# Kernel optimization log

Measured on AMD Instinct MI355X. Metric: run time of the kernel, lower is better.

Reference implementation:

```python
import jax, jax.numpy as jnp
import numpy as np

BETA = 0.25

def setup_inputs() -> dict:
    key = jax.random.key(0)
    k1, k2 = jax.random.split(key)
    N, K, D = 262144, 1024, 64
    z = jax.random.normal(k1, (N, D), dtype=jnp.float32)
    codebook = jax.random.normal(k2, (K, D), dtype=jnp.float32)
    return {"z": z, "codebook": codebook}

def reference(z, codebook):
    # Squared Euclidean distances (argmin identical to torch.cdist argmin):
    # ||z||^2 - 2 z.C^T + ||C||^2 , shape [N, K]
    z_sq = jnp.sum(z * z, axis=1, keepdims=True)            # [N,1]
    c_sq = jnp.sum(codebook * codebook, axis=1)             # [K]
    dist = z_sq - 2.0 * (z @ codebook.T) + c_sq[None, :]    # [N,K]
    indices = jnp.argmin(dist, axis=1)                      # [N] int
    z_q = codebook[indices]                                 # [N,D]
    codebook_loss = jnp.mean((jax.lax.stop_gradient(z_q) - z) ** 2)
    commitment_loss = jnp.mean((z_q - jax.lax.stop_gradient(z)) ** 2)
    vq_loss = codebook_loss + BETA * commitment_loss
    z_q_st = z + jax.lax.stop_gradient(z_q - z)             # straight-through
    return (z_q_st, vq_loss, indices, z_q)
```

## Files before the change

### kernel.cpp

```cpp
#include <hip/hip_runtime.h>
#include <hip/hip_bf16.h>

typedef __bf16 bf16x8 __attribute__((ext_vector_type(8)));
typedef float  f32x4  __attribute__((ext_vector_type(4)));

static constexpr int N_ROWS  = 262144;
static constexpr int K_CODES = 1024;
static constexpr int D_DIM   = 64;

static constexpr long LOSS_OFF = (long)N_ROWS * D_DIM;
static constexpr long IDX_OFF  = LOSS_OFF + 1;
static constexpr long ZQ_OFF   = IDX_OFF + N_ROWS;

static constexpr size_t CSQ_B   = 0;
static constexpr size_t BFRAG_B = 4096;
static constexpr size_t CNT_B   = BFRAG_B + (size_t)16 * 16384;
static constexpr size_t LIST_B  = CNT_B + 256;
static constexpr size_t PART_B  = LIST_B + (size_t)N_ROWS * 4;
static constexpr size_t WS_NEEDED = PART_B + (size_t)16384 * 4;

static constexpr int   EPI_BLOCKS = (N_ROWS * D_DIM) / (256 * 4);
static constexpr float MARGIN = 0.05f;

#define GLOAD_LDS16(g, l) __builtin_amdgcn_global_load_lds( \
    (const __attribute__((address_space(1))) unsigned int*)(g), \
    (__attribute__((address_space(3))) unsigned int*)(l), 16, 0, 0)

__global__ __launch_bounds__(256) void csq_kernel(const float* __restrict__ cb,
                                                  float* __restrict__ ws) {
    int g = blockIdx.x * 256 + threadIdx.x;
    const float4* row = reinterpret_cast<const float4*>(cb) + (size_t)g * (D_DIM / 4);
    float s = 0.f;
    #pragma unroll
    for (int j = 0; j < D_DIM / 4; ++j) {
        float4 v = row[j];
        s = fmaf(v.x, v.x, s); s = fmaf(v.y, v.y, s);
        s = fmaf(v.z, v.z, s); s = fmaf(v.w, v.w, s);
    }
    ws[g] = s;
}

__global__ __launch_bounds__(256) void prep_kernel(const float* __restrict__ cb,
                                                   char* __restrict__ wsb) {
    int t = blockIdx.x * 256 + threadIdx.x;
    int c  = t >> 3;
    int ks = (t >> 2) & 1;
    int g  = t & 3;
    const float* src = cb + (size_t)c * 64 + ks * 32 + g * 8;
    float f[8];
    #pragma unroll
    for (int i = 0; i < 8; ++i) f[i] = src[i];
    bf16x8 h, l;
    #pragma unroll
    for (int i = 0; i < 8; ++i) {
        __bf16 hv = (__bf16)f[i];
        h[i] = hv;
        l[i] = (__bf16)(f[i] - (float)hv);
    }
    int tile = c >> 6, cf = (c >> 4) & 3, n = c & 15;
    int lane = g * 16 + n;
    char* base = wsb + BFRAG_B + (size_t)tile * 16384;
    *reinterpret_cast<bf16x8*>(base + ((0 * 2 + ks) * 4 + cf) * 1024 + lane * 16) = h;
    *reinterpret_cast<bf16x8*>(base + ((1 * 2 + ks) * 4 + cf) * 1024 + lane * 16) = l;
}

__global__ __launch_bounds__(256, 2) void vq_gemm_kernel(const float* __restrict__ z,
                                                         char* __restrict__ wsb,
                                                         float* __restrict__ out) {
    __shared__ __align__(16) unsigned char sbuf[2 * 16384 + 4096];
    float* lds_csq = (float*)(sbuf + 32768);

    const int tid  = threadIdx.x;
    const int lane = tid & 63, wid = tid >> 6;
    const int l15  = lane & 15, lg = lane >> 4;

    const float* csq = (const float*)(wsb + CSQ_B);
    #pragma unroll
    for (int i = 0; i < 4; ++i) lds_csq[tid + 256 * i] = csq[tid + 256 * i];

    const int rowbase = blockIdx.x * 256 + wid * 64;
    bf16x8 ah[4][2], al[4][2];
    #pragma unroll
    for (int rf = 0; rf < 4; ++rf) {
        const float* zr = z + (size_t)(rowbase + rf * 16 + l15) * 64 + lg * 8;
        #pragma unroll
        for (int ks = 0; ks < 2; ++ks) {
            float4 a = *reinterpret_cast<const float4*>(zr + ks * 32);
            float4 b = *reinterpret_cast<const float4*>(zr + ks * 32 + 4);
            float f[8] = {a.x, a.y, a.z, a.w, b.x, b.y, b.z, b.w};
            bf16x8 h, l;
            #pragma unroll
            for (int i = 0; i < 8; ++i) {
                __bf16 hv = (__bf16)f[i];
                h[i] = hv;
                l[i] = (__bf16)(f[i] - (float)hv);
            }
            ah[rf][ks] = h; al[rf][ks] = l;
        }
    }

    float m1[16], m2[16]; int i1[16];
    #pragma unroll
    for (int s = 0; s < 16; ++s) { m1[s] = INFINITY; m2[s] = INFINITY; i1[s] = 0; }

    const char* bsrc = wsb + BFRAG_B;

    auto stage = [&](int buf, int t) {
        const char* src = bsrc + (size_t)t * 16384;
        #pragma unroll
        for (int it = 0; it < 4; ++it) {
            GLOAD_LDS16(src + it * 4096 + wid * 1024 + lane * 16,
                        sbuf + buf * 16384 + it * 4096 + wid * 1024);
        }
    };

    stage(0, 0);
    __syncthreads();

    for (int t = 0; t < 16; ++t) {
        if (t < 15) stage((t + 1) & 1, t + 1);
        const unsigned char* B = sbuf + (t & 1) * 16384;
        #pragma unroll
        for (int cf = 0; cf < 4; ++cf) {
            bf16x8 bh0 = *reinterpret_cast<const bf16x8*>(B + (0 * 4 + cf) * 1024 + lane * 16);
            bf16x8 bh1 = *reinterpret_cast<const bf16x8*>(B + (1 * 4 + cf) * 1024 + lane * 16);
            bf16x8 bl0 = *reinterpret_cast<const bf16x8*>(B + (2 * 4 + cf) * 1024 + lane * 16);
            bf16x8 bl1 = *reinterpret_cast<const bf16x8*>(B + (3 * 4 + cf) * 1024 + lane * 16);
            const int code = t * 64 + cf * 16 + l15;
            const float cq = lds_csq[code];
            #pragma unroll
            for (int rf = 0; rf < 4; ++rf) {
                f32x4 acc = {0.f, 0.f, 0.f, 0.f};
                acc = __builtin_amdgcn_mfma_f32_16x16x32_bf16(ah[rf][0], bh0, acc, 0, 0, 0);
                acc = __builtin_amdgcn_mfma_f32_16x16x32_bf16(ah[rf][1], bh1, acc, 0, 0, 0);
                acc = __builtin_amdgcn_mfma_f32_16x16x32_bf16(al[rf][0], bh0, acc, 0, 0, 0);
                acc = __builtin_amdgcn_mfma_f32_16x16x32_bf16(al[rf][1], bh1, acc, 0, 0, 0);
                acc = __builtin_amdgcn_mfma_f32_16x16x32_bf16(ah[rf][0], bl0, acc, 0, 0, 0);
                acc = __builtin_amdgcn_mfma_f32_16x16x32_bf16(ah[rf][1], bl1, acc, 0, 0, 0);
                #pragma unroll
                for (int r = 0; r < 4; ++r) {
                    float dist = fmaf(-2.f, acc[r], cq);
                    int s = rf * 4 + r;
                    bool lt = dist < m1[s];
                    m2[s] = fminf(m2[s], fmaxf(dist, m1[s]));
                    m1[s] = fminf(m1[s], dist);
                    i1[s] = lt ? code : i1[s];
                }
            }
        }
        __syncthreads();
    }

    #pragma unroll
    for (int s = 0; s < 16; ++s) {
        #pragma unroll
        for (int off = 1; off < 16; off <<= 1) {
            float om1 = __shfl_xor(m1[s], off);
            float om2 = __shfl_xor(m2[s], off);
            int   oi  = __shfl_xor(i1[s], off);
            bool lt = (om1 < m1[s]) || (om1 == m1[s] && oi < i1[s]);
            m2[s] = fminf(fminf(m2[s], om2), fmaxf(m1[s], om1));
            m1[s] = fminf(m1[s], om1);
            i1[s] = lt ? oi : i1[s];
        }
    }

    if (l15 == 0) {
        int* cnt  = (int*)(wsb + CNT_B);
        int* list = (int*)(wsb + LIST_B);
        #pragma unroll
        for (int rf = 0; rf < 4; ++rf) {
            #pragma unroll
            for (int r = 0; r < 4; ++r) {
                int s = rf * 4 + r;
                int row = rowbase + rf * 16 + lg * 4 + r;
                out[IDX_OFF + row] = (float)i1[s];
                if (m2[s] - m1[s] < MARGIN) {
                    int pos = atomicAdd(cnt, 1);
                    if (pos < N_ROWS) list[pos] = row;
                }
            }
        }
    }
}

__global__ __launch_bounds__(256) void rescore_kernel(const float* __restrict__ z,
                                                      const float* __restrict__ cb,
                                                      const char* __restrict__ wsb,
                                                      float* __restrict__ out) {
    const int lane = threadIdx.x & 63;
    const int wgid = (blockIdx.x * 256 + threadIdx.x) >> 6;
    int cnt = *(const int*)(wsb + CNT_B);
    if (cnt > N_ROWS) cnt = N_ROWS;
    const int*   list = (const int*)(wsb + LIST_B);
    const float* csq  = (const float*)(wsb + CSQ_B);

    for (int i = wgid; i < cnt; i += 256 * 4) {
        const int row = list[i];
        float4 zr[16];
        const float4* zp = reinterpret_cast<const float4*>(z) + (size_t)row * 16;
        #pragma unroll
        for (int j = 0; j < 16; ++j) zr[j] = zp[j];
        float best = INFINITY; int bi = 0;
        for (int k = lane; k < K_CODES; k += 64) {
            const float4* cp = reinterpret_cast<const float4*>(cb) + (size_t)k * 16;
            float d0 = 0.f, d1 = 0.f, d2 = 0.f, d3 = 0.f;
            #pragma unroll
            for (int j = 0; j < 16; j += 4) {
                float4 c0 = cp[j + 0], c1 = cp[j + 1], c2 = cp[j + 2], c3 = cp[j + 3];
                d0 = fmaf(zr[j+0].x, c0.x, fmaf(zr[j+0].y, c0.y, fmaf(zr[j+0].z, c0.z, fmaf(zr[j+0].w, c0.w, d0))));
                d1 = fmaf(zr[j+1].x, c1.x, fmaf(zr[j+1].y, c1.y, fmaf(zr[j+1].z, c1.z, fmaf(zr[j+1].w, c1.w, d1))));
                d2 = fmaf(zr[j+2].x, c2.x, fmaf(zr[j+2].y, c2.y, fmaf(zr[j+2].z, c2.z, fmaf(zr[j+2].w, c2.w, d2))));
                d3 = fmaf(zr[j+3].x, c3.x, fmaf(zr[j+3].y, c3.y, fmaf(zr[j+3].z, c3.z, fmaf(zr[j+3].w, c3.w, d3))));
            }
            float dot  = (d0 + d1) + (d2 + d3);
            float dist = fmaf(-2.f, dot, csq[k]);
            if (dist < best) { best = dist; bi = k; }
        }
        #pragma unroll
        for (int off = 1; off < 64; off <<= 1) {
            float ob = __shfl_xor(best, off);
            int   oi = __shfl_xor(bi, off);
            if (ob < best || (ob == best && oi < bi)) { best = ob; bi = oi; }
        }
        if (lane == 0) out[IDX_OFF + row] = (float)bi;
    }
}

__global__ __launch_bounds__(256) void argmin_old_kernel(const float* __restrict__ z,
                                                         const float* __restrict__ cb,
                                                         const float* __restrict__ ws,
                                                         float* __restrict__ out) {
    __shared__ float4 tile[64 * 16];
    __shared__ float  csq_sh[64];
    const int row = blockIdx.x * 256 + threadIdx.x;
    float4 zr[16];
    const float4* zp = reinterpret_cast<const float4*>(z) + (size_t)row * 16;
    #pragma unroll
    for (int j = 0; j < 16; ++j) zr[j] = zp[j];
    float best = __builtin_inff();
    int   bidx = 0;
    for (int k0 = 0; k0 < K_CODES; k0 += 64) {
        __syncthreads();
        const float4* src = reinterpret_cast<const float4*>(cb) + (size_t)k0 * 16;
        #pragma unroll
        for (int j = 0; j < 4; ++j)
            tile[threadIdx.x + 256 * j] = src[threadIdx.x + 256 * j];
        if (threadIdx.x < 64) csq_sh[threadIdx.x] = ws[k0 + threadIdx.x];
        __syncthreads();
        #pragma unroll 2
        for (int k = 0; k < 64; ++k) {
            float d0 = 0.f, d1 = 0.f, d2 = 0.f, d3 = 0.f;
            #pragma unroll
            for (int j = 0; j < 16; j += 4) {
                float4 c0 = tile[k*16+j+0], c1 = tile[k*16+j+1], c2 = tile[k*16+j+2], c3 = tile[k*16+j+3];
                d0 = fmaf(zr[j+0].x, c0.x, fmaf(zr[j+0].y, c0.y, fmaf(zr[j+0].z, c0.z, fmaf(zr[j+0].w, c0.w, d0))));
                d1 = fmaf(zr[j+1].x, c1.x, fmaf(zr[j+1].y, c1.y, fmaf(zr[j+1].z, c1.z, fmaf(zr[j+1].w, c1.w, d1))));
                d2 = fmaf(zr[j+2].x, c2.x, fmaf(zr[j+2].y, c2.y, fmaf(zr[j+2].z, c2.z, fmaf(zr[j+2].w, c2.w, d2))));
                d3 = fmaf(zr[j+3].x, c3.x, fmaf(zr[j+3].y, c3.y, fmaf(zr[j+3].z, c3.z, fmaf(zr[j+3].w, c3.w, d3))));
            }
            float dist = fmaf(-2.f, (d0 + d1) + (d2 + d3), csq_sh[k]);
            if (dist < best) { best = dist; bidx = k0 + k; }
        }
    }
    out[IDX_OFF + row] = (float)bidx;
}

__global__ __launch_bounds__(256) void gather_kernel(const float* __restrict__ z,
                                                     const float* __restrict__ cb,
                                                     float* __restrict__ out,
                                                     float* __restrict__ part) {
    const long g4 = (long)blockIdx.x * 256 + threadIdx.x;
    const long g  = g4 * 4;
    const int  r  = (int)(g >> 6);
    const int  d  = (int)(g & 63);

    const int k = (int)out[IDX_OFF + r];

    float4 zv = reinterpret_cast<const float4*>(z)[g4];
    float4 cv = reinterpret_cast<const float4*>(cb)[(long)k * 16 + (d >> 2)];

    float4 st;
    st.x = zv.x + (cv.x - zv.x);
    st.y = zv.y + (cv.y - zv.y);
    st.z = zv.z + (cv.z - zv.z);
    st.w = zv.w + (cv.w - zv.w);
    reinterpret_cast<float4*>(out)[g4] = st;

    float* zq = out + ZQ_OFF + g;
    zq[0] = cv.x; zq[1] = cv.y; zq[2] = cv.z; zq[3] = cv.w;

    float dx = cv.x - zv.x, dy = cv.y - zv.y, dz = cv.z - zv.z, dw = cv.w - zv.w;
    float s = fmaf(dx, dx, fmaf(dy, dy, fmaf(dz, dz, dw * dw)));

    #pragma unroll
    for (int off = 32; off > 0; off >>= 1) s += __shfl_down(s, off, 64);

    __shared__ float wsum[4];
    const int lane = threadIdx.x & 63, wid = threadIdx.x >> 6;
    if (lane == 0) wsum[wid] = s;
    __syncthreads();
    if (threadIdx.x == 0)
        part[blockIdx.x] = (wsum[0] + wsum[1]) + (wsum[2] + wsum[3]);
}

__global__ __launch_bounds__(256) void loss_kernel(const float* __restrict__ part,
                                                   float* __restrict__ out) {
    double s = 0.0;
    for (int i = threadIdx.x; i < EPI_BLOCKS; i += 256) s += (double)part[i];
    #pragma unroll
    for (int off = 32; off > 0; off >>= 1) s += __shfl_down(s, off, 64);

    __shared__ double dsum[4];
    const int lane = threadIdx.x & 63, wid = threadIdx.x >> 6;
    if (lane == 0) dsum[wid] = s;
    __syncthreads();
    if (threadIdx.x == 0) {
        double total = (dsum[0] + dsum[1]) + (dsum[2] + dsum[3]);
        out[LOSS_OFF] = (float)(1.25 * (total / (double)((long)N_ROWS * D_DIM)));
    }
}

extern "C" void kernel_launch(void* const* d_in, const int* in_sizes, int n_in,
                              void* d_out, int out_size, void* d_ws, size_t ws_size,
                              hipStream_t stream) {
    (void)in_sizes; (void)n_in; (void)out_size;
    const float* z  = (const float*)d_in[0];
    const float* cb = (const float*)d_in[1];
    float* out = (float*)d_out;
    char*  wsb = (char*)d_ws;
    float* wsf = (float*)d_ws;

    csq_kernel<<<K_CODES / 256, 256, 0, stream>>>(cb, wsf);

    if (ws_size >= WS_NEEDED) {
        hipMemsetAsync(wsb + CNT_B, 0, 4, stream);
        prep_kernel   <<<32,   256, 0, stream>>>(cb, wsb);
        vq_gemm_kernel<<<N_ROWS / 256, 256, 0, stream>>>(z, wsb, out);
        rescore_kernel<<<256,  256, 0, stream>>>(z, cb, wsb, out);
        gather_kernel <<<EPI_BLOCKS, 256, 0, stream>>>(z, cb, out, (float*)(wsb + PART_B));
        loss_kernel   <<<1,    256, 0, stream>>>((const float*)(wsb + PART_B), out);
    } else {
        argmin_old_kernel<<<N_ROWS / 256, 256, 0, stream>>>(z, cb, wsf, out);
        gather_kernel <<<EPI_BLOCKS, 256, 0, stream>>>(z, cb, out, wsf + 1024);
        loss_kernel   <<<1,    256, 0, stream>>>(wsf + 1024, out);
    }
}
```

Before: 406.9 us.

## Fuse gather and loss partials into GEMM epilogue; patch rescored rows with deltas

Moves the gather and straight-through output writes, plus the per-block squared-error partials, into the end of the GEMM argmin kernel. This removes the separate gather pass over z and the codebook. Rows that get rescored rewrite their outputs and store a loss delta (new minus old error), which the loss kernel folds in. The codebook-norm pass, counter reset and prep are merged into one kernel, and GEMM occupancy is raised to 4 blocks per SM. The GEMM kernel now carries extra LDS use and epilogue traffic, and correctness depends on the delta bookkeeping.

```diff
diff --git a/kernel.cpp b/kernel.cpp
--- a/kernel.cpp
+++ b/kernel.cpp
@@ -15,37 +15,37 @@
 static constexpr size_t CSQ_B   = 0;
 static constexpr size_t BFRAG_B = 4096;
 static constexpr size_t CNT_B   = BFRAG_B + (size_t)16 * 16384;
-static constexpr size_t LIST_B  = CNT_B + 256;
-static constexpr size_t PART_B  = LIST_B + (size_t)N_ROWS * 4;
-static constexpr size_t WS_NEEDED = PART_B + (size_t)16384 * 4;
-
+static constexpr size_t PART_B  = CNT_B + 256;
+static constexpr size_t LIST_B  = PART_B + 4096;
+static constexpr size_t WS_NEEDED = LIST_B + (size_t)N_ROWS * 4;
+
+static constexpr float MARGIN = 0.05f;
 static constexpr int   EPI_BLOCKS = (N_ROWS * D_DIM) / (256 * 4);
-static constexpr float MARGIN = 0.05f;
 
 #define GLOAD_LDS16(g, l) __builtin_amdgcn_global_load_lds( \
     (const __attribute__((address_space(1))) unsigned int*)(g), \
     (__attribute__((address_space(3))) unsigned int*)(l), 16, 0, 0)
 
-__global__ __launch_bounds__(256) void csq_kernel(const float* __restrict__ cb,
-                                                  float* __restrict__ ws) {
-    int g = blockIdx.x * 256 + threadIdx.x;
-    const float4* row = reinterpret_cast<const float4*>(cb) + (size_t)g * (D_DIM / 4);
-    float s = 0.f;
-    #pragma unroll
-    for (int j = 0; j < D_DIM / 4; ++j) {
-        float4 v = row[j];
-        s = fmaf(v.x, v.x, s); s = fmaf(v.y, v.y, s);
-        s = fmaf(v.z, v.z, s); s = fmaf(v.w, v.w, s);
-    }
-    ws[g] = s;
-}
-
-__global__ __launch_bounds__(256) void prep_kernel(const float* __restrict__ cb,
-                                                   char* __restrict__ wsb) {
-    int t = blockIdx.x * 256 + threadIdx.x;
-    int c  = t >> 3;
-    int ks = (t >> 2) & 1;
-    int g  = t & 3;
+__global__ __launch_bounds__(256) void fusedprep_kernel(const float* __restrict__ cb,
+                                                        char* __restrict__ wsb) {
+    const int t = blockIdx.x * 256 + threadIdx.x;
+    if (t == 0) *(int*)(wsb + CNT_B) = 0;
+
+    if (t < K_CODES) {
+        const float4* row = reinterpret_cast<const float4*>(cb) + (size_t)t * (D_DIM / 4);
+        float s = 0.f;
+        #pragma unroll
+        for (int j = 0; j < D_DIM / 4; ++j) {
+            float4 v = row[j];
+            s = fmaf(v.x, v.x, s); s = fmaf(v.y, v.y, s);
+            s = fmaf(v.z, v.z, s); s = fmaf(v.w, v.w, s);
+        }
+        ((float*)(wsb + CSQ_B))[t] = s;
+    }
+
+    const int c  = t >> 3;
+    const int ks = (t >> 2) & 1;
+    const int g  = t & 3;
     const float* src = cb + (size_t)c * 64 + ks * 32 + g * 8;
     float f[8];
     #pragma unroll
@@ -57,18 +57,21 @@
         h[i] = hv;
         l[i] = (__bf16)(f[i] - (float)hv);
     }
-    int tile = c >> 6, cf = (c >> 4) & 3, n = c & 15;
-    int lane = g * 16 + n;
+    const int tile = c >> 6, cf = (c >> 4) & 3, n = c & 15;
+    const int lane = g * 16 + n;
     char* base = wsb + BFRAG_B + (size_t)tile * 16384;
     *reinterpret_cast<bf16x8*>(base + ((0 * 2 + ks) * 4 + cf) * 1024 + lane * 16) = h;
     *reinterpret_cast<bf16x8*>(base + ((1 * 2 + ks) * 4 + cf) * 1024 + lane * 16) = l;
 }
 
-__global__ __launch_bounds__(256, 2) void vq_gemm_kernel(const float* __restrict__ z,
+__global__ __launch_bounds__(256, 4) void vq_gemm_kernel(const float* __restrict__ z,
+                                                         const float* __restrict__ cb,
                                                          char* __restrict__ wsb,
                                                          float* __restrict__ out) {
     __shared__ __align__(16) unsigned char sbuf[2 * 16384 + 4096];
     float* lds_csq = (float*)(sbuf + 32768);
+    int*   idx_sh  = (int*)(sbuf + 32768);
+    float* bsum    = (float*)(sbuf + 32768 + 1024);
 
     const int tid  = threadIdx.x;
     const int lane = tid & 63, wid = tid >> 6;
@@ -104,7 +107,6 @@
     for (int s = 0; s < 16; ++s) { m1[s] = INFINITY; m2[s] = INFINITY; i1[s] = 0; }
 
     const char* bsrc = wsb + BFRAG_B;
-
     auto stage = [&](int buf, int t) {
         const char* src = bsrc + (size_t)t * 16384;
         #pragma unroll
@@ -175,28 +177,51 @@
                 int s = rf * 4 + r;
                 int row = rowbase + rf * 16 + lg * 4 + r;
                 out[IDX_OFF + row] = (float)i1[s];
+                idx_sh[wid * 64 + rf * 16 + lg * 4 + r] = i1[s];
                 if (m2[s] - m1[s] < MARGIN) {
                     int pos = atomicAdd(cnt, 1);
-                    if (pos < N_ROWS) list[pos] = row;
+                    list[pos] = row;
                 }
             }
         }
     }
+    __syncthreads();
+
+    float lsum = 0.f;
+    #pragma unroll 4
+    for (int rl = 0; rl < 64; ++rl) {
+        const int row = rowbase + rl;
+        const int k   = idx_sh[wid * 64 + rl];
+        float zv = z [(size_t)row * 64 + lane];
+        float cv = cb[(size_t)k   * 64 + lane];
+        out[(size_t)row * 64 + lane]          = zv + (cv - zv);
+        out[ZQ_OFF + (size_t)row * 64 + lane] = cv;
+        float d = cv - zv;
+        lsum = fmaf(d, d, lsum);
+    }
+    #pragma unroll
+    for (int off = 32; off > 0; off >>= 1) lsum += __shfl_down(lsum, off, 64);
+    if (lane == 0) bsum[wid] = lsum;
+    __syncthreads();
+    if (tid == 0)
+        ((float*)(wsb + PART_B))[blockIdx.x] = (bsum[0] + bsum[1]) + (bsum[2] + bsum[3]);
 }
 
 __global__ __launch_bounds__(256) void rescore_kernel(const float* __restrict__ z,
                                                       const float* __restrict__ cb,
-                                                      const char* __restrict__ wsb,
+                                                      char* __restrict__ wsb,
                                                       float* __restrict__ out) {
     const int lane = threadIdx.x & 63;
     const int wgid = (blockIdx.x * 256 + threadIdx.x) >> 6;
     int cnt = *(const int*)(wsb + CNT_B);
     if (cnt > N_ROWS) cnt = N_ROWS;
-    const int*   list = (const int*)(wsb + LIST_B);
+    int*         list = (int*)(wsb + LIST_B);
     const float* csq  = (const float*)(wsb + CSQ_B);
 
     for (int i = wgid; i < cnt; i += 256 * 4) {
-        const int row = list[i];
+        const int row  = list[i];
+        const int kold = (int)out[IDX_OFF + row];
+
         float4 zr[16];
         const float4* zp = reinterpret_cast<const float4*>(z) + (size_t)row * 16;
         #pragma unroll
@@ -213,8 +238,7 @@
                 d2 = fmaf(zr[j+2].x, c2.x, fmaf(zr[j+2].y, c2.y, fmaf(zr[j+2].z, c2.z, fmaf(zr[j+2].w, c2.w, d2))));
                 d3 = fmaf(zr[j+3].x, c3.x, fmaf(zr[j+3].y, c3.y, fmaf(zr[j+3].z, c3.z, fmaf(zr[j+3].w, c3.w, d3))));
             }
-            float dot  = (d0 + d1) + (d2 + d3);
-            float dist = fmaf(-2.f, dot, csq[k]);
+            float dist = fmaf(-2.f, (d0 + d1) + (d2 + d3), csq[k]);
             if (dist < best) { best = dist; bi = k; }
         }
         #pragma unroll
@@ -223,8 +247,61 @@
             int   oi = __shfl_xor(bi, off);
             if (ob < best || (ob == best && oi < bi)) { best = ob; bi = oi; }
         }
-        if (lane == 0) out[IDX_OFF + row] = (float)bi;
-    }
+
+        float zv   = z [(size_t)row  * 64 + lane];
+        float cold = cb[(size_t)kold * 64 + lane];
+        float cnew = cb[(size_t)bi   * 64 + lane];
+        out[(size_t)row * 64 + lane]          = zv + (cnew - zv);
+        out[ZQ_OFF + (size_t)row * 64 + lane] = cnew;
+        float dn = cnew - zv, dol = cold - zv;
+        float pn = dn * dn, po = dol * dol;
+        #pragma unroll
+        for (int off = 32; off > 0; off >>= 1) {
+            pn += __shfl_down(pn, off, 64);
+            po += __shfl_down(po, off, 64);
+        }
+        if (lane == 0) {
+            out[IDX_OFF + row] = (float)bi;
+            ((float*)list)[i]  = pn - po;
+        }
+    }
+}
+
+__global__ __launch_bounds__(256) void loss_kernel(const char* __restrict__ wsb,
+                                                   float* __restrict__ out) {
+    const float* part = (const float*)(wsb + PART_B);
+    int cnt = *(const int*)(wsb + CNT_B);
+    if (cnt > N_ROWS) cnt = N_ROWS;
+    const float* delta = (const float*)(wsb + LIST_B);
+
+    double s = 0.0;
+    for (int i = threadIdx.x; i < 1024; i += 256) s += (double)part[i];
+    for (int i = threadIdx.x; i < cnt;  i += 256) s += (double)delta[i];
+    #pragma unroll
+    for (int off = 32; off > 0; off >>= 1) s += __shfl_down(s, off, 64);
+
+    __shared__ double dsum[4];
+    const int lane = threadIdx.x & 63, wid = threadIdx.x >> 6;
+    if (lane == 0) dsum[wid] = s;
+    __syncthreads();
+    if (threadIdx.x == 0) {
+        double total = (dsum[0] + dsum[1]) + (dsum[2] + dsum[3]);
+        out[LOSS_OFF] = (float)(1.25 * (total / (double)((long)N_ROWS * D_DIM)));
+    }
+}
+
+__global__ __launch_bounds__(256) void csq_kernel(const float* __restrict__ cb,
+                                                  float* __restrict__ ws) {
+    int g = blockIdx.x * 256 + threadIdx.x;
+    const float4* row = reinterpret_cast<const float4*>(cb) + (size_t)g * (D_DIM / 4);
+    float s = 0.f;
+    #pragma unroll
+    for (int j = 0; j < D_DIM / 4; ++j) {
+        float4 v = row[j];
+        s = fmaf(v.x, v.x, s); s = fmaf(v.y, v.y, s);
+        s = fmaf(v.z, v.z, s); s = fmaf(v.w, v.w, s);
+    }
+    ws[g] = s;
 }
 
 __global__ __launch_bounds__(256) void argmin_old_kernel(const float* __restrict__ z,
@@ -274,28 +351,19 @@
     const long g  = g4 * 4;
     const int  r  = (int)(g >> 6);
     const int  d  = (int)(g & 63);
-
     const int k = (int)out[IDX_OFF + r];
-
     float4 zv = reinterpret_cast<const float4*>(z)[g4];
     float4 cv = reinterpret_cast<const float4*>(cb)[(long)k * 16 + (d >> 2)];
-
     float4 st;
-    st.x = zv.x + (cv.x - zv.x);
-    st.y = zv.y + (cv.y - zv.y);
-    st.z = zv.z + (cv.z - zv.z);
-    st.w = zv.w + (cv.w - zv.w);
+    st.x = zv.x + (cv.x - zv.x); st.y = zv.y + (cv.y - zv.y);
+    st.z = zv.z + (cv.z - zv.z); st.w = zv.w + (cv.w - zv.w);
     reinterpret_cast<float4*>(out)[g4] = st;
-
     float* zq = out + ZQ_OFF + g;
     zq[0] = cv.x; zq[1] = cv.y; zq[2] = cv.z; zq[3] = cv.w;
-
     float dx = cv.x - zv.x, dy = cv.y - zv.y, dz = cv.z - zv.z, dw = cv.w - zv.w;
     float s = fmaf(dx, dx, fmaf(dy, dy, fmaf(dz, dz, dw * dw)));
-
     #pragma unroll
     for (int off = 32; off > 0; off >>= 1) s += __shfl_down(s, off, 64);
-
     __shared__ float wsum[4];
     const int lane = threadIdx.x & 63, wid = threadIdx.x >> 6;
     if (lane == 0) wsum[wid] = s;
@@ -304,13 +372,12 @@
         part[blockIdx.x] = (wsum[0] + wsum[1]) + (wsum[2] + wsum[3]);
 }
 
-__global__ __launch_bounds__(256) void loss_kernel(const float* __restrict__ part,
-                                                   float* __restrict__ out) {
+__global__ __launch_bounds__(256) void loss_old_kernel(const float* __restrict__ part,
+                                                       float* __restrict__ out) {
     double s = 0.0;
     for (int i = threadIdx.x; i < EPI_BLOCKS; i += 256) s += (double)part[i];
     #pragma unroll
     for (int off = 32; off > 0; off >>= 1) s += __shfl_down(s, off, 64);
-
     __shared__ double dsum[4];
     const int lane = threadIdx.x & 63, wid = threadIdx.x >> 6;
     if (lane == 0) dsum[wid] = s;
@@ -331,18 +398,15 @@
     char*  wsb = (char*)d_ws;
     float* wsf = (float*)d_ws;
 
-    csq_kernel<<<K_CODES / 256, 256, 0, stream>>>(cb, wsf);
-
     if (ws_size >= WS_NEEDED) {
-        hipMemsetAsync(wsb + CNT_B, 0, 4, stream);
-        prep_kernel   <<<32,   256, 0, stream>>>(cb, wsb);
-        vq_gemm_kernel<<<N_ROWS / 256, 256, 0, stream>>>(z, wsb, out);
-        rescore_kernel<<<256,  256, 0, stream>>>(z, cb, wsb, out);
-        gather_kernel <<<EPI_BLOCKS, 256, 0, stream>>>(z, cb, out, (float*)(wsb + PART_B));
-        loss_kernel   <<<1,    256, 0, stream>>>((const float*)(wsb + PART_B), out);
+        fusedprep_kernel<<<32,           256, 0, stream>>>(cb, wsb);
+        vq_gemm_kernel  <<<N_ROWS / 256, 256, 0, stream>>>(z, cb, wsb, out);
+        rescore_kernel  <<<256,          256, 0, stream>>>(z, cb, wsb, out);
+        loss_kernel     <<<1,            256, 0, stream>>>(wsb, out);
     } else {
-        argmin_old_kernel<<<N_ROWS / 256, 256, 0, stream>>>(z, cb, wsf, out);
-        gather_kernel <<<EPI_BLOCKS, 256, 0, stream>>>(z, cb, out, wsf + 1024);
-        loss_kernel   <<<1,    256, 0, stream>>>(wsf + 1024, out);
-    }
-}
+        csq_kernel       <<<K_CODES / 256, 256, 0, stream>>>(cb, wsf);
+        argmin_old_kernel<<<N_ROWS / 256,  256, 0, stream>>>(z, cb, wsf, out);
+        gather_kernel    <<<EPI_BLOCKS,    256, 0, stream>>>(z, cb, out, wsf + 1024);
+        loss_old_kernel  <<<1,             256, 0, stream>>>(wsf + 1024, out);
+    }
+}
```

After: 728.7 us. 79.1% more time.
